# Kernel tuning notes

Hardware: AMD Instinct MI355X
Metric: run time of the kernel (lower is better)

## Reference

```python
import jax, jax.numpy as jnp
import numpy as np

BETA = 0.95      # snn.Leaky(beta=0.95)
THRESHOLD = 1.0  # snntorch default
STEPS = 10


def setup_inputs() -> dict:
    key = jax.random.key(0)
    k1, k2 = jax.random.split(key)
    x = jax.random.normal(k1, (65536, 784), dtype=jnp.float32)
    # fc weight [out=10, in=784], no bias
    W = jax.random.normal(k2, (10, 784), dtype=jnp.float32) * (1.0 / np.sqrt(784.0))
    return {"x": x, "W": W}


def reference(x, W):
    # x: [B, 784] (already flat); fc(x) is the same every step -> compute once.
    cur = x @ W.T  # [B, 10]
    # snntorch Leaky (reset-by-subtraction):
    #   reset_t = spk_{t-1}; mem_t = beta*mem_{t-1} + cur - reset_t*thr; spk_t = (mem_t > thr)
    def step(carry, _):
        mem, spk = carry
        mem = BETA * mem + cur - spk * THRESHOLD
        spk = (mem > THRESHOLD).astype(cur.dtype)
        return (mem, spk), spk

    init = (jnp.zeros_like(cur), jnp.zeros_like(cur))
    _, spk_rec = jax.lax.scan(step, init, None, length=STEPS)  # [STEPS, B, 10]
    return spk_rec.sum(axis=0)  # [B, 10]
```

## Files before the change

kernel.cpp:

```cpp
#include <hip/hip_runtime.h>


constexpr int ROWS  = 65536;
constexpr int COLS  = 784;
constexpr int NOUT  = 10;
constexpr int STEPS = 10;

constexpr int BR   = 64;
constexpr int TW   = 16;
constexpr int NT   = COLS / TW;
constexpr int PADW = TW + 1;
constexpr int NH   = 8;
constexpr int CPH  = TW / NH;
constexpr int NF4  = BR * TW / 4;

__global__ void w_prep(const float* __restrict__ W, double* __restrict__ W64T) {
    int i = blockIdx.x * 256 + threadIdx.x;
    if (i < NOUT * COLS) {
        int c = i / NOUT, j = i - c * NOUT;
        W64T[i] = (double)W[(size_t)j * COLS + c];
    }
}

__global__ __launch_bounds__(512, 8)
void snn_fused(const float* __restrict__ x, const double* __restrict__ W64T,
               float* __restrict__ out) {
    __shared__ __align__(16) char smem[NH * BR * NOUT * 8];
    float*  tile = reinterpret_cast<float*>(smem);
    double* comb = reinterpret_cast<double*>(smem);

    const int tid  = threadIdx.x;
    const int r    = tid & (BR - 1);
    const int hu   = __builtin_amdgcn_readfirstlane(tid >> 6);
    const size_t row0 = (size_t)blockIdx.x * BR;

    const float* xblk = x + row0 * COLS;
    const int rr = tid >> 2, c4 = tid & 3;

    auto issue = [&](int t, float4& v) {
        if (tid < NF4)
            v = *reinterpret_cast<const float4*>(xblk + (size_t)rr * COLS + t * TW + c4 * 4);
    };
    auto wlds = [&](int b, const float4& v) {
        if (tid < NF4) {
            float* p = tile + b * (BR * PADW) + rr * PADW + c4 * 4;
            p[0] = v.x; p[1] = v.y; p[2] = v.z; p[3] = v.w;
        }
    };

    double acc[NOUT];
    #pragma unroll
    for (int j = 0; j < NOUT; ++j) acc[j] = 0.0;

    float4 rT, rA, rB, rC;
    issue(0, rT); wlds(0, rT);
    issue(1, rA);
    issue(2, rB);
    __syncthreads();

    for (int t = 0; t < NT; ++t) {
        if (t + 1 < NT) wlds((t + 1) & 1, rA);
        if (t + 3 < NT) issue(t + 3, rC);

        const float*  src = tile + (t & 1) * (BR * PADW) + r * PADW + hu * CPH;
        const double* wb  = W64T + (size_t)(t * TW + hu * CPH) * NOUT;
        #pragma unroll
        for (int c = 0; c < CPH; ++c) {
            double xd = (double)src[c];
            #pragma unroll
            for (int j = 0; j < NOUT; ++j)
                acc[j] = fma(xd, wb[c * NOUT + j], acc[j]);
        }

        __syncthreads();
        rA = rB; rB = rC;
    }

    #pragma unroll
    for (int j = 0; j < NOUT; ++j)
        comb[(hu * BR + r) * NOUT + j] = acc[j];
    __syncthreads();

    for (int i = tid; i < BR * NOUT; i += 512) {
        double c0 = comb[i]                  + comb[BR * NOUT + i];
        double c1 = comb[2 * BR * NOUT + i]  + comb[3 * BR * NOUT + i];
        double c2 = comb[4 * BR * NOUT + i]  + comb[5 * BR * NOUT + i];
        double c3 = comb[6 * BR * NOUT + i]  + comb[7 * BR * NOUT + i];
        double cur = (c0 + c1) + (c2 + c3);

        double mem = 0.0, spk = 0.0, s = 0.0;
        #pragma unroll
        for (int st = 0; st < STEPS; ++st) {
            mem = 0.95 * mem + cur - spk;
            spk = (mem > 1.0) ? 1.0 : 0.0;
            s  += spk;
        }
        out[row0 * NOUT + i] = (float)s;
    }
}

extern "C" void kernel_launch(void* const* d_in, const int* in_sizes, int n_in,
                              void* d_out, int out_size, void* d_ws, size_t ws_size,
                              hipStream_t stream) {
    const float* x = (const float*)d_in[0];
    const float* W = (const float*)d_in[1];
    float*  out  = (float*)d_out;
    double* W64T = (double*)d_ws;

    hipLaunchKernelGGL(w_prep, dim3((NOUT * COLS + 255) / 256), dim3(256), 0, stream, W, W64T);
    hipLaunchKernelGGL(snn_fused, dim3(ROWS / BR), dim3(512), 0, stream, x, W64T, out);
}
```

Measured before the change: 48.92 us.

## Stage fp64 weights in LDS per block and load two x tiles per step

Removes the separate weight-prep kernel and has each block convert and transpose W into shared memory as doubles (about 62 KB), so weight reads in the inner loop come from LDS instead of global or cache. The x tile pipeline now uses all 512 threads to load two 16-column tiles per iteration into a 4-deep LDS ring, halving the number of barriers. The larger LDS footprint lowers the launch bound to 4 blocks per CU and adds redundant per-block W conversion work.

```diff
diff --git a/kernel.cpp b/kernel.cpp
--- a/kernel.cpp
+++ b/kernel.cpp
@@ -9,41 +9,46 @@
 constexpr int BR   = 64;
 constexpr int TW   = 16;
 constexpr int NT   = COLS / TW;
-constexpr int PADW = TW + 1;
+constexpr int PADW = 17;
 constexpr int NH   = 8;
 constexpr int CPH  = TW / NH;
-constexpr int NF4  = BR * TW / 4;
 
-__global__ void w_prep(const float* __restrict__ W, double* __restrict__ W64T) {
-    int i = blockIdx.x * 256 + threadIdx.x;
-    if (i < NOUT * COLS) {
-        int c = i / NOUT, j = i - c * NOUT;
-        W64T[i] = (double)W[(size_t)j * COLS + c];
-    }
-}
+constexpr int XBUF_F  = BR * PADW;
+constexpr int W_OFF_B = 4 * XBUF_F * 4;
+constexpr int LDS_B   = W_OFF_B + NOUT * COLS * 8;
 
-__global__ __launch_bounds__(512, 8)
-void snn_fused(const float* __restrict__ x, const double* __restrict__ W64T,
+__global__ __launch_bounds__(512, 4)
+void snn_fused(const float* __restrict__ x, const float* __restrict__ W,
                float* __restrict__ out) {
-    __shared__ __align__(16) char smem[NH * BR * NOUT * 8];
-    float*  tile = reinterpret_cast<float*>(smem);
+    __shared__ __align__(16) char smem[LDS_B];
+    float*  xb   = reinterpret_cast<float*>(smem);
+    double* wl   = reinterpret_cast<double*>(smem + W_OFF_B);
     double* comb = reinterpret_cast<double*>(smem);
 
-    const int tid  = threadIdx.x;
-    const int r    = tid & (BR - 1);
-    const int hu   = __builtin_amdgcn_readfirstlane(tid >> 6);
+    const int tid = threadIdx.x;
+    const int r   = tid & 63;
+    const int hu  = __builtin_amdgcn_readfirstlane(tid >> 6);
     const size_t row0 = (size_t)blockIdx.x * BR;
+    const float* xblk = x + row0 * COLS;
 
-    const float* xblk = x + row0 * COLS;
-    const int rr = tid >> 2, c4 = tid & 3;
+    for (int i = tid; i < NOUT * COLS; i += 512) {
+        int c = i / NOUT, j = i - c * NOUT;
+        wl[i] = (double)W[(size_t)j * COLS + c];
+    }
 
-    auto issue = [&](int t, float4& v) {
-        if (tid < NF4)
+    const int s   = tid >> 8;
+    const int idx = tid & 255;
+    const int rr  = idx >> 2, c4 = idx & 3;
+
+    auto issuePair = [&](int t0, float4& v) {
+        int t = t0 + s;
+        if (t < NT)
             v = *reinterpret_cast<const float4*>(xblk + (size_t)rr * COLS + t * TW + c4 * 4);
     };
-    auto wlds = [&](int b, const float4& v) {
-        if (tid < NF4) {
-            float* p = tile + b * (BR * PADW) + rr * PADW + c4 * 4;
+    auto wldsPair = [&](int t0, const float4& v) {
+        int t = t0 + s;
+        if (t < NT) {
+            float* p = xb + (t & 3) * XBUF_F + rr * PADW + c4 * 4;
             p[0] = v.x; p[1] = v.y; p[2] = v.z; p[3] = v.w;
         }
     };
@@ -52,18 +57,37 @@
     #pragma unroll
     for (int j = 0; j < NOUT; ++j) acc[j] = 0.0;
 
-    float4 rT, rA, rB, rC;
-    issue(0, rT); wlds(0, rT);
-    issue(1, rA);
-    issue(2, rB);
+    float4 pA, pB, pC;
+    issuePair(0, pA); wldsPair(0, pA);
+    issuePair(2, pB);
     __syncthreads();
 
-    for (int t = 0; t < NT; ++t) {
-        if (t + 1 < NT) wlds((t + 1) & 1, rA);
-        if (t + 3 < NT) issue(t + 3, rC);
+    for (int p = 0; p < NT / 2; ++p) {
+        const int t = 2 * p;
+        wldsPair(t + 2, pB);
+        issuePair(t + 4, pC);
 
-        const float*  src = tile + (t & 1) * (BR * PADW) + r * PADW + hu * CPH;
-        const double* wb  = W64T + (size_t)(t * TW + hu * CPH) * NOUT;
+        #pragma unroll
+        for (int u = 0; u < 2; ++u) {
+            const int tt = t + u;
+            const float*  src = xb + (tt & 3) * XBUF_F + r * PADW + hu * CPH;
+            const double* wb  = wl + (size_t)(tt * TW + hu * CPH) * NOUT;
+            #pragma unroll
+            for (int c = 0; c < CPH; ++c) {
+                double xd = (double)src[c];
+                #pragma unroll
+                for (int j = 0; j < NOUT; ++j)
+                    acc[j] = fma(xd, wb[c * NOUT + j], acc[j]);
+            }
+        }
+        __syncthreads();
+        pB = pC;
+    }
+
+    {
+        const int tt = NT - 1;
+        const float*  src = xb + (tt & 3) * XBUF_F + r * PADW + hu * CPH;
+        const double* wb  = wl + (size_t)(tt * TW + hu * CPH) * NOUT;
         #pragma unroll
         for (int c = 0; c < CPH; ++c) {
             double xd = (double)src[c];
@@ -71,10 +95,8 @@
             for (int j = 0; j < NOUT; ++j)
                 acc[j] = fma(xd, wb[c * NOUT + j], acc[j]);
         }
-
-        __syncthreads();
-        rA = rB; rB = rC;
     }
+    __syncthreads();
 
     #pragma unroll
     for (int j = 0; j < NOUT; ++j)
@@ -88,14 +110,14 @@
         double c3 = comb[6 * BR * NOUT + i]  + comb[7 * BR * NOUT + i];
         double cur = (c0 + c1) + (c2 + c3);
 
-        double mem = 0.0, spk = 0.0, s = 0.0;
+        double mem = 0.0, spk = 0.0, sum = 0.0;
         #pragma unroll
         for (int st = 0; st < STEPS; ++st) {
             mem = 0.95 * mem + cur - spk;
             spk = (mem > 1.0) ? 1.0 : 0.0;
-            s  += spk;
+            sum += spk;
         }
-        out[row0 * NOUT + i] = (float)s;
+        out[row0 * NOUT + i] = (float)sum;
     }
 }
 
@@ -104,9 +126,6 @@
                               hipStream_t stream) {
     const float* x = (const float*)d_in[0];
     const float* W = (const float*)d_in[1];
-    float*  out  = (float*)d_out;
-    double* W64T = (double*)d_ws;
-
-    hipLaunchKernelGGL(w_prep, dim3((NOUT * COLS + 255) / 256), dim3(256), 0, stream, W, W64T);
-    hipLaunchKernelGGL(snn_fused, dim3(ROWS / BR), dim3(512), 0, stream, x, W64T, out);
+    float* out = (float*)d_out;
+    hipLaunchKernelGGL(snn_fused, dim3(ROWS / BR), dim3(512), 0, stream, x, W, out);
 }
```

Result: slower. 57.00 us (+16.5%).
